# Kernel tuning notes

Measured on AMD Instinct MI355X. Metric: run time of the kernel, lower is better.

Reference implementation:

```python
import jax, jax.numpy as jnp
import numpy as np

KEEP_RATIO = 0.25
BLOCK = 8
TEMP = 0.1


def setup_inputs() -> dict:
    key = jax.random.key(0)
    features = jax.random.normal(key, (8, 256, 132, 132), dtype=jnp.float32)
    return {"features": features, "enabled": 1}


def reference(features, enabled):
    B, C, H, W = features.shape
    if not enabled:
        return jnp.ones((B, C, H, W), dtype=features.dtype)
    # pad H, W up to multiples of BLOCK (zeros, like F.pad default)
    ph = (-H) % BLOCK
    pw = (-W) % BLOCK
    x = jnp.pad(jnp.abs(features), ((0, 0), (0, 0), (0, ph), (0, pw)))
    Hp, Wp = H + ph, W + pw
    nh, nw = Hp // BLOCK, Wp // BLOCK
    # avg_pool2d(kernel=stride=BLOCK) == block-mean via reshape
    pooled = x.reshape(B, C, nh, BLOCK, nw, BLOCK).mean(axis=(3, 5))  # [B,C,nh,nw]
    total = nh * nw
    scores = pooled.reshape(B, C, total)
    keep = max(1, min(total, int(round(total * KEEP_RATIO))))
    top_vals, top_idx = jax.lax.top_k(scores, keep)  # sorted descending, like torch.topk
    # hard mask: scatter ones at topk indices
    flat_idx = top_idx.reshape(B * C, keep)
    hard = (jnp.zeros((B * C, total), dtype=features.dtype)
            .at[jnp.arange(B * C)[:, None], flat_idx].set(1.0)
            .reshape(B, C, total))
    # training-mode straight-through soft blend
    thr = jax.lax.stop_gradient(top_vals[..., -1:])  # kth value as threshold
    soft = jax.nn.sigmoid((scores - thr) / TEMP)
    soft = soft * (keep / jnp.maximum(soft.sum(-1, keepdims=True), 1e-6))
    soft = jnp.clip(soft, 0.0, 1.0)
    mask = jax.lax.stop_gradient(hard) - jax.lax.stop_gradient(soft) + soft
    # upsample blocks back to pixels (repeat_interleave) and crop padding
    block_mask = mask.reshape(B, C, nh, nw)
    full = jnp.repeat(jnp.repeat(block_mask, BLOCK, axis=2), BLOCK, axis=3)
    return full[:, :, :H, :W]
```

## Files before the change

### kernel.cpp

```cpp
#include <hip/hip_runtime.h>


#define HH 132
#define WW 132
#define NB 17
#define TOTAL 289
#define NPAD 320
#define KEEP 72
#define NTHREADS 256
#define NV ((HH * WW) / 4)

typedef float floatx4 __attribute__((ext_vector_type(4)));

__global__ __launch_bounds__(NTHREADS)
void gate_kernel(const float4* __restrict__ feats4,
                 const int* __restrict__ enabled_p,
                 float4* __restrict__ out4) {
    const int plane = blockIdx.x;
    const int t = threadIdx.x;
    const float4* __restrict__ fp = feats4 + (size_t)plane * NV;
    floatx4* __restrict__ op = (floatx4*)(out4 + (size_t)plane * NV);

    __shared__ __align__(16) double   s_score[NPAD];
    __shared__ __align__(16) unsigned s_key[NPAD];
    __shared__ float s_hard[TOTAL];

    for (int b = t; b < TOTAL; b += NTHREADS) {
        const int br = b / NB;
        const int bc = b - br * NB;
        const int nr = (br == NB - 1) ? 4 : 8;
        const int hc = (bc == NB - 1) ? 1 : 2;
        const float4* bp = fp + br * (8 * 33) + bc * 2;
        double a0 = 0.0, a1 = 0.0;
        #pragma unroll
        for (int rr = 0; rr < 8; ++rr) {
            if (rr < nr) {
                const float4 x = bp[rr * 33];
                a0 += (double)fabsf(x.x) + (double)fabsf(x.y)
                    + (double)fabsf(x.z) + (double)fabsf(x.w);
                if (hc == 2) {
                    const float4 y = bp[rr * 33 + 1];
                    a1 += (double)fabsf(y.x) + (double)fabsf(y.y)
                        + (double)fabsf(y.z) + (double)fabsf(y.w);
                }
            }
        }
        s_score[b] = a0 + a1;
    }
    if (t < NPAD - TOTAL) s_score[TOTAL + t] = 0.0;
    __syncthreads();

    for (int i = t; i < NPAD; i += NTHREADS) {
        s_key[i] = (unsigned)((unsigned long long)
                       __double_as_longlong(s_score[i]) >> 32);
    }
    __syncthreads();

    const int en = *enabled_p;
    const uint4* __restrict__ sk4 = (const uint4*)s_key;
    for (int i = t; i < TOTAL; i += NTHREADS) {
        const unsigned ki = s_key[i];
        int r = 0, e = 0;
        #pragma unroll 10
        for (int q = 0; q < NPAD / 4; ++q) {
            const uint4 k = sk4[q];
            r += (int)(k.x > ki) + (int)(k.y > ki)
               + (int)(k.z > ki) + (int)(k.w > ki);
            e += (int)(k.x == ki) + (int)(k.y == ki)
               + (int)(k.z == ki) + (int)(k.w == ki);
        }
        int rank = r;
        if (e > 1) {
            const double si = s_score[i];
            rank = 0;
            for (int j = 0; j < TOTAL; ++j) {
                const double sj = s_score[j];
                rank += (int)((sj > si) || ((sj == si) && (j < i)));
            }
        }
        s_hard[i] = (!en || rank < KEEP) ? 1.0f : 0.0f;
    }
    __syncthreads();

    for (int v = t; v < NV; v += NTHREADS) {
        const int base = v * 4;
        const int row = base / WW;
        const int col = base - row * WW;
        const float m = s_hard[(row >> 3) * NB + (col >> 3)];
        const floatx4 mv = {m, m, m, m};
        __builtin_nontemporal_store(mv, &op[v]);
    }
}

extern "C" void kernel_launch(void* const* d_in, const int* in_sizes, int n_in,
                              void* d_out, int out_size, void* d_ws, size_t ws_size,
                              hipStream_t stream) {
    const float4* feats = (const float4*)d_in[0];
    const int* enabled = (const int*)d_in[1];
    float4* out = (float4*)d_out;
    const int planes = 8 * 256;
    gate_kernel<<<planes, NTHREADS, 0, stream>>>(feats, enabled, out);
}
```

Measured before the change: 278.0 us.

## Split gating into score and write kernels with coalesced LDS-atomic pooling

Pooling now reads the input fully coalesced. Each thread walks float4s linearly and accumulates into per-block scores with shared-memory double atomics, instead of one thread striding rows per 8x8 block. When workspace is available the work splits into two kernels: a score/rank kernel that writes a byte mask to workspace, and a separate kernel that expands the mask to the output. This separates the read-heavy and write-heavy phases at the cost of an extra launch and a small workspace round trip. The fallback monolithic kernel uses the same coalesced pooling, but double atomics in LDS may be slow on contended addresses.

```diff
diff --git a/kernel.cpp b/kernel.cpp
--- a/kernel.cpp
+++ b/kernel.cpp
@@ -7,15 +7,94 @@
 #define TOTAL 289
 #define NPAD 320
 #define KEEP 72
-#define NTHREADS 256
 #define NV ((HH * WW) / 4)
+#define PLANES 2048
 
 typedef float floatx4 __attribute__((ext_vector_type(4)));
 
-__global__ __launch_bounds__(NTHREADS)
-void gate_kernel(const float4* __restrict__ feats4,
-                 const int* __restrict__ enabled_p,
-                 float4* __restrict__ out4) {
+__global__ __launch_bounds__(NPAD)
+void gate_score(const float4* __restrict__ feats4,
+                const int* __restrict__ enabled_p,
+                unsigned char* __restrict__ ws_mask) {
+    const int plane = blockIdx.x;
+    const int t = threadIdx.x;
+    const float4* __restrict__ fp = feats4 + (size_t)plane * NV;
+
+    __shared__ __align__(16) double   s_score[NPAD];
+    __shared__ __align__(16) unsigned s_key[NPAD];
+
+    s_score[t] = 0.0;
+    __syncthreads();
+
+    for (int v = t; v < NV; v += NPAD) {
+        const float4 x = fp[v];
+        const double s = (double)fabsf(x.x) + (double)fabsf(x.y)
+                       + (double)fabsf(x.z) + (double)fabsf(x.w);
+        const int base = v * 4;
+        const int row = base / WW;
+        const int col = base - row * WW;
+        atomicAdd(&s_score[(row >> 3) * NB + (col >> 3)], s);
+    }
+    __syncthreads();
+
+    s_key[t] = (unsigned)((unsigned long long)
+                   __double_as_longlong(s_score[t]) >> 32);
+    __syncthreads();
+
+    const int en = *enabled_p;
+    if (t < TOTAL) {
+        const unsigned ki = s_key[t];
+        const uint4* __restrict__ sk4 = (const uint4*)s_key;
+        int r = 0, e = 0;
+        #pragma unroll 10
+        for (int q = 0; q < NPAD / 4; ++q) {
+            const uint4 k = sk4[q];
+            r += (int)(k.x > ki) + (int)(k.y > ki)
+               + (int)(k.z > ki) + (int)(k.w > ki);
+            e += (int)(k.x == ki) + (int)(k.y == ki)
+               + (int)(k.z == ki) + (int)(k.w == ki);
+        }
+        int rank = r;
+        if (e > 1) {
+            const double si = s_score[t];
+            rank = 0;
+            for (int j = 0; j < TOTAL; ++j) {
+                const double sj = s_score[j];
+                rank += (int)((sj > si) || ((sj == si) && (j < t)));
+            }
+        }
+        ws_mask[(size_t)plane * TOTAL + t] =
+            (unsigned char)((!en || rank < KEEP) ? 1 : 0);
+    }
+}
+
+#define NTB 256
+__global__ __launch_bounds__(NTB)
+void gate_write(const unsigned char* __restrict__ ws_mask,
+                float4* __restrict__ out4) {
+    const int plane = blockIdx.x;
+    const int t = threadIdx.x;
+    floatx4* __restrict__ op = (floatx4*)(out4 + (size_t)plane * NV);
+
+    __shared__ float s_hard[TOTAL];
+    const unsigned char* __restrict__ mp = ws_mask + (size_t)plane * TOTAL;
+    for (int i = t; i < TOTAL; i += NTB) s_hard[i] = (float)mp[i];
+    __syncthreads();
+
+    for (int v = t; v < NV; v += NTB) {
+        const int base = v * 4;
+        const int row = base / WW;
+        const int col = base - row * WW;
+        const float m = s_hard[(row >> 3) * NB + (col >> 3)];
+        const floatx4 mv = {m, m, m, m};
+        __builtin_nontemporal_store(mv, &op[v]);
+    }
+}
+
+__global__ __launch_bounds__(NTB)
+void gate_mono(const float4* __restrict__ feats4,
+               const int* __restrict__ enabled_p,
+               float4* __restrict__ out4) {
     const int plane = blockIdx.x;
     const int t = threadIdx.x;
     const float4* __restrict__ fp = feats4 + (size_t)plane * NV;
@@ -25,40 +104,25 @@
     __shared__ __align__(16) unsigned s_key[NPAD];
     __shared__ float s_hard[TOTAL];
 
-    for (int b = t; b < TOTAL; b += NTHREADS) {
-        const int br = b / NB;
-        const int bc = b - br * NB;
-        const int nr = (br == NB - 1) ? 4 : 8;
-        const int hc = (bc == NB - 1) ? 1 : 2;
-        const float4* bp = fp + br * (8 * 33) + bc * 2;
-        double a0 = 0.0, a1 = 0.0;
-        #pragma unroll
-        for (int rr = 0; rr < 8; ++rr) {
-            if (rr < nr) {
-                const float4 x = bp[rr * 33];
-                a0 += (double)fabsf(x.x) + (double)fabsf(x.y)
-                    + (double)fabsf(x.z) + (double)fabsf(x.w);
-                if (hc == 2) {
-                    const float4 y = bp[rr * 33 + 1];
-                    a1 += (double)fabsf(y.x) + (double)fabsf(y.y)
-                        + (double)fabsf(y.z) + (double)fabsf(y.w);
-                }
-            }
-        }
-        s_score[b] = a0 + a1;
+    for (int i = t; i < NPAD; i += NTB) s_score[i] = 0.0;
+    __syncthreads();
+    for (int v = t; v < NV; v += NTB) {
+        const float4 x = fp[v];
+        const double s = (double)fabsf(x.x) + (double)fabsf(x.y)
+                       + (double)fabsf(x.z) + (double)fabsf(x.w);
+        const int base = v * 4;
+        const int row = base / WW;
+        const int col = base - row * WW;
+        atomicAdd(&s_score[(row >> 3) * NB + (col >> 3)], s);
     }
-    if (t < NPAD - TOTAL) s_score[TOTAL + t] = 0.0;
     __syncthreads();
-
-    for (int i = t; i < NPAD; i += NTHREADS) {
+    for (int i = t; i < NPAD; i += NTB)
         s_key[i] = (unsigned)((unsigned long long)
                        __double_as_longlong(s_score[i]) >> 32);
-    }
     __syncthreads();
-
     const int en = *enabled_p;
     const uint4* __restrict__ sk4 = (const uint4*)s_key;
-    for (int i = t; i < TOTAL; i += NTHREADS) {
+    for (int i = t; i < TOTAL; i += NTB) {
         const unsigned ki = s_key[i];
         int r = 0, e = 0;
         #pragma unroll 10
@@ -81,8 +145,7 @@
         s_hard[i] = (!en || rank < KEEP) ? 1.0f : 0.0f;
     }
     __syncthreads();
-
-    for (int v = t; v < NV; v += NTHREADS) {
+    for (int v = t; v < NV; v += NTB) {
         const int base = v * 4;
         const int row = base / WW;
         const int col = base - row * WW;
@@ -98,6 +161,12 @@
     const float4* feats = (const float4*)d_in[0];
     const int* enabled = (const int*)d_in[1];
     float4* out = (float4*)d_out;
-    const int planes = 8 * 256;
-    gate_kernel<<<planes, NTHREADS, 0, stream>>>(feats, enabled, out);
+    const size_t need = (size_t)PLANES * TOTAL;
+    if (d_ws != nullptr && ws_size >= need) {
+        unsigned char* mask = (unsigned char*)d_ws;
+        gate_score<<<PLANES, NPAD, 0, stream>>>(feats, enabled, mask);
+        gate_write<<<PLANES, NTB, 0, stream>>>(mask, out);
+    } else {
+        gate_mono<<<PLANES, NTB, 0, stream>>>(feats, enabled, out);
+    }
 }
```

Result: no change. 278.9 us (+0.3%).
